# Kernel tuning notes

Measured on AMD Instinct MI355X. Metric: run time of the kernel, lower is better.

The kernel has to match this reference:

```python
import jax, jax.numpy as jnp
import numpy as np

SPATIAL_SHAPES = [(128, 128), (64, 64), (32, 32), (16, 16)]  # sum HW = 21760
N_HEADS, N_LEVELS, N_POINTS, EMBED = 8, 4, 4, 256
HEAD_D = EMBED // N_HEADS
B, NQ = 2, 10000
NV = sum(h * w for h, w in SPATIAL_SHAPES)


def setup_inputs() -> dict:
    key = jax.random.key(0)
    ks = jax.random.split(key, 12)
    s = 0.02
    return {
        "query": jax.random.normal(ks[0], (B, NQ, EMBED), jnp.float32),
        "key": jax.random.normal(ks[1], (B, NV, EMBED), jnp.float32),
        "value": jax.random.normal(ks[2], (B, NV, EMBED), jnp.float32),
        "W_off": jax.random.normal(ks[3], (EMBED, N_HEADS * N_LEVELS * N_POINTS * 2), jnp.float32) * s,
        "b_off": jax.random.uniform(ks[4], (N_HEADS * N_LEVELS * N_POINTS * 2,), jnp.float32, -0.9, 0.9),
        "W_attn": jax.random.normal(ks[5], (EMBED, N_HEADS * N_LEVELS * N_POINTS), jnp.float32) * s,
        "b_attn": jnp.zeros((N_HEADS * N_LEVELS * N_POINTS,), jnp.float32),
        "W_v": jax.random.normal(ks[6], (EMBED, EMBED), jnp.float32) * s,
        "b_v": jnp.zeros((EMBED,), jnp.float32),
        "W_out": jax.random.normal(ks[7], (EMBED, EMBED), jnp.float32) * s,
        "b_out": jnp.zeros((EMBED,), jnp.float32),
    }


def bilinear_sample(img, gx, gy):
    """img: [N, Hs, Ws, C]; gx, gy: [N, P] in [-1, 1].
    Torch grid_sample semantics: bilinear, align_corners=True, padding_mode='zeros'.
    gx indexes width, gy indexes height."""
    N, Hs, Ws, C = img.shape
    px = (gx + 1.0) * 0.5 * (Ws - 1)
    py = (gy + 1.0) * 0.5 * (Hs - 1)
    x0 = jnp.floor(px)
    y0 = jnp.floor(py)
    wx = (px - x0)[..., None]
    wy = (py - y0)[..., None]
    x0i = x0.astype(jnp.int32)
    y0i = y0.astype(jnp.int32)
    flat = img.reshape(N, Hs * Ws, C)

    def gather(xi, yi):
        valid = ((xi >= 0) & (xi < Ws) & (yi >= 0) & (yi < Hs))[..., None]
        xc = jnp.clip(xi, 0, Ws - 1)
        yc = jnp.clip(yi, 0, Hs - 1)
        idx = yc * Ws + xc  # [N, P]
        v = jnp.take_along_axis(flat, idx[..., None], axis=1)  # [N, P, C]
        return jnp.where(valid, v, 0.0)

    v00 = gather(x0i, y0i)
    v01 = gather(x0i + 1, y0i)
    v10 = gather(x0i, y0i + 1)
    v11 = gather(x0i + 1, y0i + 1)
    top = v00 * (1.0 - wx) + v01 * wx
    bot = v10 * (1.0 - wx) + v11 * wx
    return top * (1.0 - wy) + bot * wy


def reference(query, key, value, W_off, b_off, W_attn, b_attn, W_v, b_v, W_out, b_out):
    Bq, Nq, _ = query.shape
    # value projection -> per-head values
    v = (value @ W_v + b_v).reshape(Bq, NV, N_HEADS, HEAD_D)
    # sampling locations (used directly as normalized [-1,1] grid coords) and weights
    off = (query @ W_off + b_off).reshape(Bq, Nq, N_HEADS, N_LEVELS, N_POINTS, 2)
    attn = (query @ W_attn + b_attn).reshape(Bq, Nq, N_HEADS, N_LEVELS, N_POINTS)
    attn = jax.nn.softmax(attn, axis=-1)  # softmax over points per level (as in source)

    out = jnp.zeros((Bq, Nq, EMBED), query.dtype)
    start = 0
    for lvl, (Hs, Ws) in enumerate(SPATIAL_SHAPES):
        vl = v[:, start:start + Hs * Ws].reshape(Bq, Hs, Ws, N_HEADS, HEAD_D)
        start += Hs * Ws
        vl = vl.transpose(0, 3, 1, 2, 4).reshape(Bq * N_HEADS, Hs, Ws, HEAD_D)
        gl = off[:, :, :, lvl]  # [B, Nq, H, P, 2]
        gl = gl.transpose(0, 2, 1, 3, 4).reshape(Bq * N_HEADS, Nq * N_POINTS, 2)
        samp = bilinear_sample(vl, gl[..., 0], gl[..., 1])  # [B*H, Nq*P, D]
        samp = samp.reshape(Bq, N_HEADS, Nq, N_POINTS, HEAD_D)
        wl = attn[:, :, :, lvl].transpose(0, 2, 1, 3)  # [B, H, Nq, P]
        out = out + jnp.einsum('bhqp,bhqpd->bqhd', wl, samp).reshape(Bq, Nq, EMBED)
    return out @ W_out + b_out
```

## Files before the change

kernel.cpp:

```cpp
#include <hip/hip_runtime.h>
#include <math.h>

#define B_   2
#define NQ_  10000
#define NV_  21760
#define EMB  256
#define MQ   (B_*NQ_)
#define MV   (B_*NV_)

typedef short bf16x8 __attribute__((ext_vector_type(8)));
typedef float f32x4  __attribute__((ext_vector_type(4)));

__device__ constexpr int LSc[4] = {0, 16384, 20480, 21504};

__device__ __forceinline__ unsigned short f2bf(float x) {
  unsigned u = __builtin_bit_cast(unsigned, x);
  u += 0x7FFFu + ((u >> 16) & 1u);
  return (unsigned short)(u >> 16);
}
__device__ __forceinline__ float bf2f(unsigned short s) {
  return __builtin_bit_cast(float, (unsigned)s << 16);
}

__global__ __launch_bounds__(256) void prep_weights(
    const float* __restrict__ Wv, const float* __restrict__ Wattn,
    const float* __restrict__ Woff, const float* __restrict__ Wout,
    unsigned short* __restrict__ WvT, unsigned short* __restrict__ WoutT,
    unsigned short* __restrict__ WqHi, unsigned short* __restrict__ WqLo) {
  int n = blockIdx.x;
  int k = threadIdx.x;
  if (n < 256) {
    WvT[n * 256 + k] = f2bf(Wv[k * 256 + n]);
  } else if (n < 512) {
    int c = n - 256;
    WoutT[c * 256 + k] = f2bf(Wout[k * 256 + c]);
  } else {
    int qr = n - 512;
    float x = (qr < 256) ? Woff[k * 256 + qr] : Wattn[k * 128 + (qr - 256)];
    unsigned short hi = f2bf(x);
    WqHi[qr * 256 + k] = hi;
    WqLo[qr * 256 + k] = f2bf(x - bf2f(hi));
  }
}

template <int MODE, typename OutT, bool VPERM = false>
__global__ __launch_bounds__(256) void gemm_mfma(
    const void* __restrict__ Aa,
    const unsigned short* __restrict__ Bt, const unsigned short* __restrict__ Bt2,
    const float* __restrict__ bias, const float* __restrict__ bias2,
    OutT* __restrict__ C, float* __restrict__ C2, int M, int N) {
  constexpr int BM = 128, BK = 32;
  __shared__ unsigned short As[(MODE == 3 ? 2 : 1) * BM * BK];
  __shared__ unsigned short Bs[(MODE == 3 ? 2 : 1) * BM * BK];
  unsigned short* As2 = As + BM * BK;
  unsigned short* Bs2 = Bs + BM * BK;

  const int tid = threadIdx.x;
  const int lane = tid & 63, wv = tid >> 6;
  const int wr = wv >> 1, wc = wv & 1;
  const int row0 = blockIdx.x * BM, col0 = blockIdx.y * BM;

  auto lds_addr = [](int row, int kslot) -> int {
    return row * 64 + ((kslot ^ ((row >> 1) & 3)) << 4);
  };

  auto stage_bf = [&](unsigned short* dst, const unsigned short* src,
                      int rbase, int rmax, int kk) {
#pragma unroll
    for (int i = 0; i < 2; ++i) {
      int idx = tid + 256 * i;
      int row = idx >> 2, ks = idx & 3;
      int rg = min(rbase + row, rmax);
      bf16x8 vdat = *(const bf16x8*)(src + (size_t)rg * 256 + kk + ks * 8);
      *(bf16x8*)((char*)dst + lds_addr(row, ks)) = vdat;
    }
  };
  auto stage_cvt = [&](unsigned short* dst, const float* src,
                       int rbase, int rmax, int kk) {
#pragma unroll
    for (int i = 0; i < 4; ++i) {
      int idx = tid + 256 * i;
      int row = idx >> 3, c4 = idx & 7;
      int rg = min(rbase + row, rmax);
      float4 vdat = *(const float4*)(src + (size_t)rg * 256 + kk + c4 * 4);
      ushort4 o;
      o.x = f2bf(vdat.x); o.y = f2bf(vdat.y);
      o.z = f2bf(vdat.z); o.w = f2bf(vdat.w);
      *(ushort4*)((char*)dst + lds_addr(row, c4 >> 1) + (c4 & 1) * 8) = o;
    }
  };
  auto stage_cvt2 = [&](unsigned short* dstH, unsigned short* dstL,
                        const float* src, int rbase, int rmax, int kk) {
#pragma unroll
    for (int i = 0; i < 4; ++i) {
      int idx = tid + 256 * i;
      int row = idx >> 3, c4 = idx & 7;
      int rg = min(rbase + row, rmax);
      float4 vdat = *(const float4*)(src + (size_t)rg * 256 + kk + c4 * 4);
      ushort4 hh, ll;
      hh.x = f2bf(vdat.x); ll.x = f2bf(vdat.x - bf2f(hh.x));
      hh.y = f2bf(vdat.y); ll.y = f2bf(vdat.y - bf2f(hh.y));
      hh.z = f2bf(vdat.z); ll.z = f2bf(vdat.z - bf2f(hh.z));
      hh.w = f2bf(vdat.w); ll.w = f2bf(vdat.w - bf2f(hh.w));
      int a = lds_addr(row, c4 >> 1) + (c4 & 1) * 8;
      *(ushort4*)((char*)dstH + a) = hh;
      *(ushort4*)((char*)dstL + a) = ll;
    }
  };

  const bool three_term = (MODE == 3) && (col0 < 256);

  f32x4 acc[4][4] = {};

  for (int kk = 0; kk < 256; kk += BK) {
    if (kk) __syncthreads();
    if constexpr (MODE == 1)
      stage_cvt(As, (const float*)Aa, row0, M - 1, kk);
    else if constexpr (MODE == 3) {
      if (three_term)
        stage_cvt2(As, As2, (const float*)Aa, row0, M - 1, kk);
      else
        stage_cvt(As, (const float*)Aa, row0, M - 1, kk);
    } else
      stage_bf(As, (const unsigned short*)Aa, row0, M - 1, kk);
    stage_bf(Bs, Bt, col0, N - 1, kk);
    if constexpr (MODE == 3)
      if (three_term) stage_bf(Bs2, Bt2, col0, N - 1, kk);
    __syncthreads();

    const int kslot = lane >> 4;
    bf16x8 af[4], bfr[4];
#pragma unroll
    for (int i = 0; i < 4; ++i) {
      int ra = wr * 64 + i * 16 + (lane & 15);
      af[i] = *(const bf16x8*)((const char*)As + lds_addr(ra, kslot));
      int rb = wc * 64 + i * 16 + (lane & 15);
      bfr[i] = *(const bf16x8*)((const char*)Bs + lds_addr(rb, kslot));
    }
#pragma unroll
    for (int mi = 0; mi < 4; ++mi)
#pragma unroll
      for (int ni = 0; ni < 4; ++ni)
        acc[mi][ni] = __builtin_amdgcn_mfma_f32_16x16x32_bf16(
            af[mi], bfr[ni], acc[mi][ni], 0, 0, 0);

    if constexpr (MODE == 3) {
      if (three_term) {
        bf16x8 af2[4], bfr2[4];
#pragma unroll
        for (int i = 0; i < 4; ++i) {
          int ra = wr * 64 + i * 16 + (lane & 15);
          af2[i] = *(const bf16x8*)((const char*)As2 + lds_addr(ra, kslot));
          int rb = wc * 64 + i * 16 + (lane & 15);
          bfr2[i] = *(const bf16x8*)((const char*)Bs2 + lds_addr(rb, kslot));
        }
#pragma unroll
        for (int mi = 0; mi < 4; ++mi)
#pragma unroll
          for (int ni = 0; ni < 4; ++ni) {
            acc[mi][ni] = __builtin_amdgcn_mfma_f32_16x16x32_bf16(
                af2[mi], bfr[ni], acc[mi][ni], 0, 0, 0);
            acc[mi][ni] = __builtin_amdgcn_mfma_f32_16x16x32_bf16(
                af[mi], bfr2[ni], acc[mi][ni], 0, 0, 0);
          }
      }
    }
  }

  if constexpr (VPERM) {
    float bb4[4];
#pragma unroll
    for (int ni = 0; ni < 4; ++ni)
      bb4[ni] = bias[col0 + wc * 64 + ni * 16 + (lane & 15)];
#pragma unroll
    for (int mi = 0; mi < 4; ++mi) {
#pragma unroll
      for (int r = 0; r < 4; ++r) {
        int row = row0 + wr * 64 + mi * 16 + ((lane >> 4) << 2) + r;
        int pix = row, bb2 = 0;
        if (pix >= NV_) { bb2 = 1; pix -= NV_; }
        int lvl = (pix >= 16384) + (pix >= 20480) + (pix >= 21504);
        int sh = 7 - lvl;
        int rel = pix - LSc[lvl];
        int x = rel & ((1 << sh) - 1), y = rel >> sh;
        unsigned pairoff = ((unsigned)((y << (sh - 1)) + (x >> 1)) << 10) |
                           ((unsigned)(x & 1) << 3);
        char* vout = (char*)C + ((size_t)bb2 * NV_ + LSc[lvl]) * 512 + pairoff;
#pragma unroll
        for (int ni = 0; ni < 4; ++ni) {
          int gcol = col0 + wc * 64 + ni * 16 + (lane & 15);
          float val = acc[mi][ni][r] + bb4[ni];
          int h = gcol >> 5, d = gcol & 31;
          *(unsigned short*)(vout + h * 128 + (d >> 2) * 16 + (d & 3) * 2) =
              f2bf(val);
        }
      }
    }
  } else {
#pragma unroll
    for (int ni = 0; ni < 4; ++ni) {
      int gcol = col0 + wc * 64 + ni * 16 + (lane & 15);
      float bb = (MODE == 3 && gcol >= 256) ? bias2[gcol - 256] : bias[gcol];
#pragma unroll
      for (int mi = 0; mi < 4; ++mi) {
        int rowbase = row0 + wr * 64 + mi * 16 + ((lane >> 4) << 2);
        f32x4 a = acc[mi][ni];
#pragma unroll
        for (int r = 0; r < 4; ++r) {
          int row = rowbase + r;
          if (row < M) {
            float val = a[r] + bb;
            if constexpr (MODE == 3) {
              if (gcol >= 256)
                C2[(size_t)row * 128 + (gcol - 256)] = val;
              else
                C[(size_t)row * 256 + gcol] = (OutT)val;
            } else if constexpr (sizeof(OutT) == 2) {
              C[(size_t)row * N + gcol] = (OutT)f2bf(val);
            } else {
              C[(size_t)row * N + gcol] = (OutT)val;
            }
          }
        }
      }
    }
  }
}

__global__ __launch_bounds__(512) void msda_sample7(
    const char* __restrict__ v,
    const float* __restrict__ off,
    const float* __restrict__ attnlg,
    ushort4* __restrict__ tmp4) {
  __shared__ unsigned coeff[4 * 136 * 8];
  const int tid = threadIdx.x;
  const int lane = tid & 63;
  const int wid = tid >> 6;
  const int wq = wid >> 1;
  const int w = wid & 1;
  const int bq = blockIdx.x * 4 + wq;
  const int b = (blockIdx.x * 4) / NQ_;

  unsigned* cbase = coeff + wq * (136 * 8);
  const float* offq = off + (size_t)bq * 256;
  const float* attq = attnlg + (size_t)bq * 128;

  {
    int h = lane >> 3, dl = (lane >> 2) & 1, p = lane & 3;
    int l = 2 * w + dl;
    int Wl = 128 >> l, sh = 7 - l;

    const float* lg = attq + h * 16 + l * 4;
    float l0 = lg[0], l1 = lg[1], l2 = lg[2], l3 = lg[3];
    float m = fmaxf(fmaxf(l0, l1), fmaxf(l2, l3));
    float e0 = expf(l0 - m), e1 = expf(l1 - m);
    float e2 = expf(l2 - m), e3 = expf(l3 - m);
    float ep = (p == 0) ? e0 : (p == 1) ? e1 : (p == 2) ? e2 : e3;
    float wsm = ep / (e0 + e1 + e2 + e3);

    float gx = offq[h * 32 + (l * 4 + p) * 2 + 0];
    float gy = offq[h * 32 + (l * 4 + p) * 2 + 1];
    float s = 0.5f * (float)(Wl - 1);
    float px = fmaf(gx, s, s), py = fmaf(gy, s, s);
    float x0f = floorf(px), y0f = floorf(py);
    float wx = px - x0f, wy = py - y0f;
    int x0 = (int)x0f, y0 = (int)y0f;

    bool bx0 = (unsigned)x0 < (unsigned)Wl, bx1 = (unsigned)(x0 + 1) < (unsigned)Wl;
    bool by0 = (unsigned)y0 < (unsigned)Wl, by1 = (unsigned)(y0 + 1) < (unsigned)Wl;
    int x0c = min(max(x0, 0), Wl - 1), x1c = min(max(x0 + 1, 0), Wl - 1);
    int y0c = min(max(y0, 0), Wl - 1), y1c = min(max(y0 + 1, 0), Wl - 1);

    auto poff = [&](int xx, int yy) -> unsigned {
      return ((unsigned)((yy << (sh - 1)) + (xx >> 1)) << 10) |
             ((unsigned)(xx & 1) << 3);
    };

    float wxm = 1.f - wx, wym = 1.f - wy;
    float w00 = (bx0 & by0) ? wsm * wxm * wym : 0.f;
    float w01 = (bx1 & by0) ? wsm * wx  * wym : 0.f;
    float w10 = (bx0 & by1) ? wsm * wxm * wy  : 0.f;
    float w11 = (bx1 & by1) ? wsm * wx  * wy  : 0.f;

    unsigned* slot = cbase + (h * 17 + l * 4 + p) * 8;
    uint4 s0;
    s0.x = poff(x0c, y0c);
    s0.y = poff(x1c, y0c);
    s0.z = poff(x0c, y1c);
    s0.w = poff(x1c, y1c);
    *(uint4*)slot = s0;
    uint4 s1;
    s1.x = __builtin_bit_cast(unsigned, w00);
    s1.y = __builtin_bit_cast(unsigned, w01);
    s1.z = __builtin_bit_cast(unsigned, w10);
    s1.w = __builtin_bit_cast(unsigned, w11);
    *(uint4*)(slot + 4) = s1;
  }
  __syncthreads();

  const int h = lane >> 3, c4 = lane & 7;
  const unsigned laneoff = (unsigned)(h * 128 + c4 * 16);
  float4 acc = make_float4(0.f, 0.f, 0.f, 0.f);

#pragma unroll
  for (int dl = 0; dl < 2; ++dl) {
    const int l = 2 * w + dl;
    const char* lb = v + ((size_t)b * NV_ + LSc[l]) * 512;
    const unsigned* cb = cbase + (h * 17 + l * 4) * 8;
#pragma unroll
    for (int p = 0; p < 4; ++p) {
      uint4 s0 = *(const uint4*)(cb + p * 8);
      uint4 s1 = *(const uint4*)(cb + p * 8 + 4);
      float w00 = __builtin_bit_cast(float, s1.x);
      float w01 = __builtin_bit_cast(float, s1.y);
      float w10 = __builtin_bit_cast(float, s1.z);
      float w11 = __builtin_bit_cast(float, s1.w);

      uint2 r00 = *(const uint2*)(lb + (laneoff + s0.x));
      uint2 r01 = *(const uint2*)(lb + (laneoff + s0.y));
      uint2 r10 = *(const uint2*)(lb + (laneoff + s0.z));
      uint2 r11 = *(const uint2*)(lb + (laneoff + s0.w));

      acc.x += w00 * __builtin_bit_cast(float, r00.x << 16)
             + w01 * __builtin_bit_cast(float, r01.x << 16)
             + w10 * __builtin_bit_cast(float, r10.x << 16)
             + w11 * __builtin_bit_cast(float, r11.x << 16);
      acc.y += w00 * __builtin_bit_cast(float, r00.x & 0xFFFF0000u)
             + w01 * __builtin_bit_cast(float, r01.x & 0xFFFF0000u)
             + w10 * __builtin_bit_cast(float, r10.x & 0xFFFF0000u)
             + w11 * __builtin_bit_cast(float, r11.x & 0xFFFF0000u);
      acc.z += w00 * __builtin_bit_cast(float, r00.y << 16)
             + w01 * __builtin_bit_cast(float, r01.y << 16)
             + w10 * __builtin_bit_cast(float, r10.y << 16)
             + w11 * __builtin_bit_cast(float, r11.y << 16);
      acc.w += w00 * __builtin_bit_cast(float, r00.y & 0xFFFF0000u)
             + w01 * __builtin_bit_cast(float, r01.y & 0xFFFF0000u)
             + w10 * __builtin_bit_cast(float, r10.y & 0xFFFF0000u)
             + w11 * __builtin_bit_cast(float, r11.y & 0xFFFF0000u);
    }
  }

  __syncthreads();
  float4* red = (float4*)coeff;
  if (w == 1) red[wq * 64 + lane] = acc;
  __syncthreads();
  if (w == 0) {
    float4 o2 = red[wq * 64 + lane];
    acc.x += o2.x; acc.y += o2.y; acc.z += o2.z; acc.w += o2.w;
    ushort4 o;
    o.x = f2bf(acc.x); o.y = f2bf(acc.y); o.z = f2bf(acc.z); o.w = f2bf(acc.w);
    tmp4[(size_t)bq * 64 + lane] = o;
  }
}

extern "C" void kernel_launch(void* const* d_in, const int* in_sizes, int n_in,
                              void* d_out, int out_size, void* d_ws, size_t ws_size,
                              hipStream_t stream) {
  const float* query  = (const float*)d_in[0];
  const float* value  = (const float*)d_in[2];
  const float* W_off  = (const float*)d_in[3];
  const float* b_off  = (const float*)d_in[4];
  const float* W_attn = (const float*)d_in[5];
  const float* b_attn = (const float*)d_in[6];
  const float* W_v    = (const float*)d_in[7];
  const float* b_v    = (const float*)d_in[8];
  const float* W_out  = (const float*)d_in[9];
  const float* b_out  = (const float*)d_in[10];
  float* out = (float*)d_out;

  char* p = (char*)d_ws;
  unsigned short* v_bf  = (unsigned short*)p; p += (size_t)MV * 256 * 2;
  float*          off_w = (float*)p;          p += (size_t)MQ * 256 * 4;
  float*          att_w = (float*)p;          p += (size_t)MQ * 128 * 4;
  unsigned short* tmp_bf= (unsigned short*)p; p += (size_t)MQ * 256 * 2;
  unsigned short* WvT   = (unsigned short*)p; p += 256 * 256 * 2;
  unsigned short* WoutT = (unsigned short*)p; p += 256 * 256 * 2;
  unsigned short* WqHi  = (unsigned short*)p; p += 384 * 256 * 2;
  unsigned short* WqLo  = (unsigned short*)p; p += 384 * 256 * 2;

  prep_weights<<<dim3(896), dim3(256), 0, stream>>>(
      W_v, W_attn, W_off, W_out, WvT, WoutT, WqHi, WqLo);

  gemm_mfma<1, unsigned short, true><<<dim3(MV / 128, 2), dim3(256), 0, stream>>>(
      value, WvT, nullptr, b_v, nullptr, v_bf, nullptr, MV, 256);

  gemm_mfma<3, float><<<dim3((MQ + 127) / 128, 3), dim3(256), 0, stream>>>(
      query, WqHi, WqLo, b_off, b_attn, off_w, att_w, MQ, 384);

  msda_sample7<<<dim3(MQ / 4), dim3(512), 0, stream>>>(
      (const char*)v_bf, off_w, att_w, (ushort4*)tmp_bf);

  gemm_mfma<0, float><<<dim3((MQ + 127) / 128, 2), dim3(256), 0, stream>>>(
      tmp_bf, WoutT, nullptr, b_out, nullptr, out, nullptr, MQ, 256);
}
```

Baseline: 125.3 us.

## Widen value layout to 16-byte gathers and stage VPERM epilogue through LDS

The packed bf16 value layout changes so each lane fetches 8 channels (16 bytes) per bilinear corner instead of 4. In the sampler, each wave now covers two points at once, split across its two half-waves, and the halves are merged with a cross-lane shuffle. The value-projection GEMM epilogue now writes its permuted tile into shared memory first, then stores it to global with coalesced 16-byte writes instead of scattered 2-byte stores. This reduces gather instruction count and scattered global writes, at the cost of extra LDS traffic, syncs and a larger shared buffer.

```diff
diff --git a/kernel.cpp b/kernel.cpp
--- a/kernel.cpp
+++ b/kernel.cpp
@@ -50,10 +50,12 @@
     const float* __restrict__ bias, const float* __restrict__ bias2,
     OutT* __restrict__ C, float* __restrict__ C2, int M, int N) {
   constexpr int BM = 128, BK = 32;
-  __shared__ unsigned short As[(MODE == 3 ? 2 : 1) * BM * BK];
-  __shared__ unsigned short Bs[(MODE == 3 ? 2 : 1) * BM * BK];
-  unsigned short* As2 = As + BM * BK;
-  unsigned short* Bs2 = Bs + BM * BK;
+  constexpr int SMEM_SHORTS = (MODE == 3 || VPERM) ? 16384 : 8192;
+  __shared__ unsigned short smem[SMEM_SHORTS];
+  unsigned short* As  = smem;
+  unsigned short* Bs  = smem + ((MODE == 3) ? 2 : 1) * BM * BK;
+  unsigned short* As2 = smem + BM * BK;
+  unsigned short* Bs2 = smem + 3 * BM * BK;
 
   const int tid = threadIdx.x;
   const int lane = tid & 63, wv = tid >> 6;
@@ -172,29 +174,38 @@
 #pragma unroll
     for (int ni = 0; ni < 4; ++ni)
       bb4[ni] = bias[col0 + wc * 64 + ni * 16 + (lane & 15)];
+    __syncthreads();
+    unsigned short* pbuf = smem;
 #pragma unroll
     for (int mi = 0; mi < 4; ++mi) {
 #pragma unroll
       for (int r = 0; r < 4; ++r) {
-        int row = row0 + wr * 64 + mi * 16 + ((lane >> 4) << 2) + r;
-        int pix = row, bb2 = 0;
-        if (pix >= NV_) { bb2 = 1; pix -= NV_; }
-        int lvl = (pix >= 16384) + (pix >= 20480) + (pix >= 21504);
-        int sh = 7 - lvl;
-        int rel = pix - LSc[lvl];
-        int x = rel & ((1 << sh) - 1), y = rel >> sh;
-        unsigned pairoff = ((unsigned)((y << (sh - 1)) + (x >> 1)) << 10) |
-                           ((unsigned)(x & 1) << 3);
-        char* vout = (char*)C + ((size_t)bb2 * NV_ + LSc[lvl]) * 512 + pairoff;
+        int lr = wr * 64 + mi * 16 + ((lane >> 4) << 2) + r;
+        int pb = lr >> 1, par = lr & 1;
 #pragma unroll
         for (int ni = 0; ni < 4; ++ni) {
-          int gcol = col0 + wc * 64 + ni * 16 + (lane & 15);
+          int lcol = wc * 64 + ni * 16 + (lane & 15);
           float val = acc[mi][ni][r] + bb4[ni];
-          int h = gcol >> 5, d = gcol & 31;
-          *(unsigned short*)(vout + h * 128 + (d >> 2) * 16 + (d & 3) * 2) =
-              f2bf(val);
+          int hl = lcol >> 5, d = lcol & 31;
+          int off = pb * 512 + hl * 128 + ((d >> 3) << 5) + (par << 4) +
+                    ((d & 7) << 1);
+          *(unsigned short*)((char*)pbuf + off) = f2bf(val);
         }
       }
+    }
+    __syncthreads();
+    int pix0 = row0, bb2 = 0;
+    if (pix0 >= NV_) { bb2 = 1; pix0 -= NV_; }
+    int lvl = (pix0 >= 16384) + (pix0 >= 20480) + (pix0 >= 21504);
+    int rel0 = pix0 - LSc[lvl];
+    char* dst = (char*)C + ((size_t)bb2 * NV_ + LSc[lvl]) * 512 +
+                (size_t)(rel0 >> 1) * 1024 + (size_t)(col0 >> 5) * 128;
+    int pb = tid >> 2, q = tid & 3;
+#pragma unroll
+    for (int i = 0; i < 8; ++i) {
+      int u = q * 16 + i * 64;
+      uint4 vd = *(const uint4*)((const char*)pbuf + pb * 512 + u);
+      *(uint4*)(dst + (size_t)pb * 1024 + u) = vd;
     }
   } else {
 #pragma unroll
@@ -227,11 +238,11 @@
   }
 }
 
-__global__ __launch_bounds__(512) void msda_sample7(
+__global__ __launch_bounds__(512) void msda_sample8(
     const char* __restrict__ v,
     const float* __restrict__ off,
     const float* __restrict__ attnlg,
-    ushort4* __restrict__ tmp4) {
+    uint4* __restrict__ tmp4) {
   __shared__ unsigned coeff[4 * 136 * 8];
   const int tid = threadIdx.x;
   const int lane = tid & 63;
@@ -273,7 +284,7 @@
 
     auto poff = [&](int xx, int yy) -> unsigned {
       return ((unsigned)((yy << (sh - 1)) + (xx >> 1)) << 10) |
-             ((unsigned)(xx & 1) << 3);
+             ((unsigned)(xx & 1) << 4);
     };
 
     float wxm = 1.f - wx, wym = 1.f - wy;
@@ -282,7 +293,7 @@
     float w10 = (bx0 & by1) ? wsm * wxm * wy  : 0.f;
     float w11 = (bx1 & by1) ? wsm * wx  * wy  : 0.f;
 
-    unsigned* slot = cbase + (h * 17 + l * 4 + p) * 8;
+    unsigned* slot = cbase + ((h * 17 + l * 4 + p)) * 8;
     uint4 s0;
     s0.x = poff(x0c, y0c);
     s0.y = poff(x1c, y0c);
@@ -298,58 +309,91 @@
   }
   __syncthreads();
 
-  const int h = lane >> 3, c4 = lane & 7;
-  const unsigned laneoff = (unsigned)(h * 128 + c4 * 16);
-  float4 acc = make_float4(0.f, 0.f, 0.f, 0.f);
+  const int pslot = lane >> 5;
+  const int h = (lane >> 2) & 7;
+  const int cq = lane & 3;
+  const unsigned laneoff = (unsigned)(h * 128 + cq * 32);
+  float4 a0 = make_float4(0.f, 0.f, 0.f, 0.f);
+  float4 a1 = make_float4(0.f, 0.f, 0.f, 0.f);
 
 #pragma unroll
   for (int dl = 0; dl < 2; ++dl) {
     const int l = 2 * w + dl;
     const char* lb = v + ((size_t)b * NV_ + LSc[l]) * 512;
-    const unsigned* cb = cbase + (h * 17 + l * 4) * 8;
-#pragma unroll
-    for (int p = 0; p < 4; ++p) {
-      uint4 s0 = *(const uint4*)(cb + p * 8);
-      uint4 s1 = *(const uint4*)(cb + p * 8 + 4);
+#pragma unroll
+    for (int piter = 0; piter < 2; ++piter) {
+      const int p = piter * 2 + pslot;
+      const unsigned* cb = cbase + (h * 17 + l * 4 + p) * 8;
+      uint4 s0 = *(const uint4*)cb;
+      uint4 s1 = *(const uint4*)(cb + 4);
       float w00 = __builtin_bit_cast(float, s1.x);
       float w01 = __builtin_bit_cast(float, s1.y);
       float w10 = __builtin_bit_cast(float, s1.z);
       float w11 = __builtin_bit_cast(float, s1.w);
 
-      uint2 r00 = *(const uint2*)(lb + (laneoff + s0.x));
-      uint2 r01 = *(const uint2*)(lb + (laneoff + s0.y));
-      uint2 r10 = *(const uint2*)(lb + (laneoff + s0.z));
-      uint2 r11 = *(const uint2*)(lb + (laneoff + s0.w));
-
-      acc.x += w00 * __builtin_bit_cast(float, r00.x << 16)
-             + w01 * __builtin_bit_cast(float, r01.x << 16)
-             + w10 * __builtin_bit_cast(float, r10.x << 16)
-             + w11 * __builtin_bit_cast(float, r11.x << 16);
-      acc.y += w00 * __builtin_bit_cast(float, r00.x & 0xFFFF0000u)
-             + w01 * __builtin_bit_cast(float, r01.x & 0xFFFF0000u)
-             + w10 * __builtin_bit_cast(float, r10.x & 0xFFFF0000u)
-             + w11 * __builtin_bit_cast(float, r11.x & 0xFFFF0000u);
-      acc.z += w00 * __builtin_bit_cast(float, r00.y << 16)
-             + w01 * __builtin_bit_cast(float, r01.y << 16)
-             + w10 * __builtin_bit_cast(float, r10.y << 16)
-             + w11 * __builtin_bit_cast(float, r11.y << 16);
-      acc.w += w00 * __builtin_bit_cast(float, r00.y & 0xFFFF0000u)
-             + w01 * __builtin_bit_cast(float, r01.y & 0xFFFF0000u)
-             + w10 * __builtin_bit_cast(float, r10.y & 0xFFFF0000u)
-             + w11 * __builtin_bit_cast(float, r11.y & 0xFFFF0000u);
-    }
-  }
+      uint4 r00 = *(const uint4*)(lb + (laneoff + s0.x));
+      uint4 r01 = *(const uint4*)(lb + (laneoff + s0.y));
+      uint4 r10 = *(const uint4*)(lb + (laneoff + s0.z));
+      uint4 r11 = *(const uint4*)(lb + (laneoff + s0.w));
+
+      a0.x += w00 * __builtin_bit_cast(float, r00.x << 16)
+            + w01 * __builtin_bit_cast(float, r01.x << 16)
+            + w10 * __builtin_bit_cast(float, r10.x << 16)
+            + w11 * __builtin_bit_cast(float, r11.x << 16);
+      a0.y += w00 * __builtin_bit_cast(float, r00.x & 0xFFFF0000u)
+            + w01 * __builtin_bit_cast(float, r01.x & 0xFFFF0000u)
+            + w10 * __builtin_bit_cast(float, r10.x & 0xFFFF0000u)
+            + w11 * __builtin_bit_cast(float, r11.x & 0xFFFF0000u);
+      a0.z += w00 * __builtin_bit_cast(float, r00.y << 16)
+            + w01 * __builtin_bit_cast(float, r01.y << 16)
+            + w10 * __builtin_bit_cast(float, r10.y << 16)
+            + w11 * __builtin_bit_cast(float, r11.y << 16);
+      a0.w += w00 * __builtin_bit_cast(float, r00.y & 0xFFFF0000u)
+            + w01 * __builtin_bit_cast(float, r01.y & 0xFFFF0000u)
+            + w10 * __builtin_bit_cast(float, r10.y & 0xFFFF0000u)
+            + w11 * __builtin_bit_cast(float, r11.y & 0xFFFF0000u);
+      a1.x += w00 * __builtin_bit_cast(float, r00.z << 16)
+            + w01 * __builtin_bit_cast(float, r01.z << 16)
+            + w10 * __builtin_bit_cast(float, r10.z << 16)
+            + w11 * __builtin_bit_cast(float, r11.z << 16);
+      a1.y += w00 * __builtin_bit_cast(float, r00.z & 0xFFFF0000u)
+            + w01 * __builtin_bit_cast(float, r01.z & 0xFFFF0000u)
+            + w10 * __builtin_bit_cast(float, r10.z & 0xFFFF0000u)
+            + w11 * __builtin_bit_cast(float, r11.z & 0xFFFF0000u);
+      a1.z += w00 * __builtin_bit_cast(float, r00.w << 16)
+            + w01 * __builtin_bit_cast(float, r01.w << 16)
+            + w10 * __builtin_bit_cast(float, r10.w << 16)
+            + w11 * __builtin_bit_cast(float, r11.w << 16);
+      a1.w += w00 * __builtin_bit_cast(float, r00.w & 0xFFFF0000u)
+            + w01 * __builtin_bit_cast(float, r01.w & 0xFFFF0000u)
+            + w10 * __builtin_bit_cast(float, r10.w & 0xFFFF0000u)
+            + w11 * __builtin_bit_cast(float, r11.w & 0xFFFF0000u);
+    }
+  }
+
+  a0.x += __shfl_xor(a0.x, 32); a0.y += __shfl_xor(a0.y, 32);
+  a0.z += __shfl_xor(a0.z, 32); a0.w += __shfl_xor(a0.w, 32);
+  a1.x += __shfl_xor(a1.x, 32); a1.y += __shfl_xor(a1.y, 32);
+  a1.z += __shfl_xor(a1.z, 32); a1.w += __shfl_xor(a1.w, 32);
 
   __syncthreads();
   float4* red = (float4*)coeff;
-  if (w == 1) red[wq * 64 + lane] = acc;
+  if (w == 1 && lane < 32) {
+    red[(wq * 32 + lane) * 2 + 0] = a0;
+    red[(wq * 32 + lane) * 2 + 1] = a1;
+  }
   __syncthreads();
-  if (w == 0) {
-    float4 o2 = red[wq * 64 + lane];
-    acc.x += o2.x; acc.y += o2.y; acc.z += o2.z; acc.w += o2.w;
-    ushort4 o;
-    o.x = f2bf(acc.x); o.y = f2bf(acc.y); o.z = f2bf(acc.z); o.w = f2bf(acc.w);
-    tmp4[(size_t)bq * 64 + lane] = o;
+  if (w == 0 && lane < 32) {
+    float4 o0 = red[(wq * 32 + lane) * 2 + 0];
+    float4 o1 = red[(wq * 32 + lane) * 2 + 1];
+    a0.x += o0.x; a0.y += o0.y; a0.z += o0.z; a0.w += o0.w;
+    a1.x += o1.x; a1.y += o1.y; a1.z += o1.z; a1.w += o1.w;
+    uint4 o;
+    o.x = (unsigned)f2bf(a0.x) | ((unsigned)f2bf(a0.y) << 16);
+    o.y = (unsigned)f2bf(a0.z) | ((unsigned)f2bf(a0.w) << 16);
+    o.z = (unsigned)f2bf(a1.x) | ((unsigned)f2bf(a1.y) << 16);
+    o.w = (unsigned)f2bf(a1.z) | ((unsigned)f2bf(a1.w) << 16);
+    *(uint4*)((char*)tmp4 + (size_t)bq * 512 + h * 64 + cq * 16) = o;
   }
 }
 
@@ -387,8 +431,8 @@
   gemm_mfma<3, float><<<dim3((MQ + 127) / 128, 3), dim3(256), 0, stream>>>(
       query, WqHi, WqLo, b_off, b_attn, off_w, att_w, MQ, 384);
 
-  msda_sample7<<<dim3(MQ / 4), dim3(512), 0, stream>>>(
-      (const char*)v_bf, off_w, att_w, (ushort4*)tmp_bf);
+  msda_sample8<<<dim3(MQ / 4), dim3(512), 0, stream>>>(
+      (const char*)v_bf, off_w, att_w, (uint4*)tmp_bf);
 
   gemm_mfma<0, float><<<dim3((MQ + 127) / 128, 2), dim3(256), 0, stream>>>(
       tmp_bf, WoutT, nullptr, b_out, nullptr, out, nullptr, MQ, 256);
```

Result: slower. 132.6 us (+5.8%).
